# Kernel tuning notes

Hardware: AMD Instinct MI355X
Metric: run time of the kernel (lower is better)

Reference implementation:

```python
import jax, jax.numpy as jnp
import numpy as np

F_IN, F_H, N_A, N_B = 256, 512, 40, 4
N_GRAPHS, NODES_PER_GRAPH = 4096, 32
N_NODES = N_GRAPHS * NODES_PER_GRAPH
D_OUT = N_B + N_B * N_A  # 164
BN_EPS = 1e-5


def setup_inputs() -> dict:
    key = jax.random.key(0)
    ks = jax.random.split(key, 8)
    X = jax.random.normal(ks[0], (N_NODES, F_IN), dtype=jnp.float32)
    # fixed-size graphs: consistent NX / NX_rep pair
    NX = jnp.full((N_GRAPHS,), NODES_PER_GRAPH, dtype=jnp.int64)
    NX_rep = jnp.repeat(jnp.arange(N_GRAPHS, dtype=jnp.int64), NODES_PER_GRAPH)
    def kaiming(k, fo, fi):
        return jax.random.normal(k, (fo, fi), dtype=jnp.float32) * np.float32(1.0 / np.sqrt(fi))
    return {
        "X": X, "NX": NX, "NX_rep": NX_rep,
        "W_h": kaiming(ks[1], F_H, 2 * F_IN),          # linear_h (no bias)
        "g_h": jnp.ones((F_H,), jnp.float32), "b_h": jnp.zeros((F_H,), jnp.float32),
        "W_ht": kaiming(ks[2], F_H, F_IN),              # linear_h_t (no bias)
        "g_ht": jnp.ones((F_H,), jnp.float32), "b_ht": jnp.zeros((F_H,), jnp.float32),
        "W_x": kaiming(ks[3], D_OUT, F_H) * 0.1,        # linear_x
        "b_x": jnp.zeros((D_OUT,), jnp.float32),
        "W_xt": kaiming(ks[4], 1, F_H) * 0.1,           # linear_x_t
        "b_xt": jnp.zeros((1,), jnp.float32),
    }


def _batchnorm(x, gamma, beta):
    # BatchNorm1d in training mode: batch statistics, biased variance
    mean = jnp.mean(x, axis=0)
    var = jnp.var(x, axis=0)
    return (x - mean) * jax.lax.rsqrt(var + BN_EPS) * gamma + beta


def reference(X, NX, NX_rep, W_h, g_h, b_h, W_ht, g_ht, b_ht, W_x, b_x, W_xt, b_xt):
    n_graphs = NX.shape[0]
    # graph-level mean pooling via segment sum  -> [G, F_in]
    X_end = jax.ops.segment_sum(X, NX_rep, num_segments=n_graphs) / NX[:, None].astype(X.dtype)
    # concat node features with gathered graph context -> [N, 2*F_in]
    Xc = jnp.concatenate([X, X_end[NX_rep]], axis=1)
    X_h = jax.nn.relu(_batchnorm(Xc @ W_h.T, g_h, b_h))          # [N, F_h]
    X_h_end = jax.nn.relu(_batchnorm(X_end @ W_ht.T, g_ht, b_ht))  # [G, F_h]
    X_x = jnp.exp(X_h @ W_x.T + b_x)                              # [N, D_OUT]
    X_x_end = jnp.exp(X_h_end @ W_xt.T + b_xt)                    # [G, 1]
    # segmented softmax denominator (per graph, over all nodes x D_OUT + end logit)
    X_sum = jnp.sum(jax.ops.segment_sum(X_x, NX_rep, num_segments=n_graphs),
                    axis=-1, keepdims=True) + X_x_end             # [G, 1]
    X_softmax = X_x / X_sum[NX_rep]                               # [N, D_OUT]
    X_softmax_end = X_x_end / X_sum                               # [G, 1]
    connect = X_softmax[:, :N_B]                                  # [N, N_B]
    append = X_softmax[:, N_B:].reshape(-1, N_A, N_B)             # [N, N_A, N_B]
    end = X_softmax_end.squeeze(-1)                               # [G]
    return (append, connect, end)
```

## Files before the change

### kernel.cpp

```cpp
#include <hip/hip_runtime.h>
#include <hip/hip_bf16.h>

typedef __hip_bfloat16 bf16;
typedef __attribute__((ext_vector_type(8))) short bf16x8;
typedef __attribute__((ext_vector_type(4))) float f32x4;

#define N_NODES   131072
#define N_GRAPHS  4096
#define FIN       256
#define FH        512
#define NPAD      176
#define NREAL     164

#define OFF_XENDB  0UL
#define OFF_W1A    2097152UL
#define OFF_BCAT   2359296UL
#define OFF_WXB    2883584UL
#define OFF_STATS  3063808UL
#define OFF_XXE    3072000UL
#define OFF_CCAT   3088384UL
#define OFF_H      19865600UL

__device__ __forceinline__ void gld_lds16(const void* g, void* l) {
  __builtin_amdgcn_global_load_lds(
      (const __attribute__((address_space(1))) void*)g,
      (__attribute__((address_space(3))) void*)l, 16, 0, 0);
}

__device__ __forceinline__ float bf2f(unsigned short u) {
  unsigned int x = ((unsigned int)u) << 16; float f;
  __builtin_memcpy(&f, &x, 4); return f;
}
__device__ __forceinline__ unsigned short f2bf(float f) {
  bf16 h = __float2bfloat16(f); unsigned short u;
  __builtin_memcpy(&u, &h, 2); return u;
}

__global__ __launch_bounds__(256) void k_wcast(
    const float* __restrict__ W_h, const float* __restrict__ W_ht,
    const float* __restrict__ W_x,
    bf16* __restrict__ W1a, bf16* __restrict__ Bcat, bf16* __restrict__ Wxb,
    float* __restrict__ stats)
{
  int i = blockIdx.x * 256 + threadIdx.x;
  if (i < 2048) stats[i] = 0.f;
  if (i < 512 * 512) {
    int of = i >> 9, ic = i & 511;
    float v = W_h[i];
    if (ic < 256) W1a[of * 256 + ic] = __float2bfloat16(v);
    else          Bcat[of * 256 + (ic - 256)] = __float2bfloat16(v);
  }
  if (i < 512 * 256) Bcat[512 * 256 + i] = __float2bfloat16(W_ht[i]);
  if (i < NPAD * 512) {
    int n = i >> 9;
    Wxb[i] = (n < NREAL) ? __float2bfloat16(W_x[i]) : __float2bfloat16(0.f);
  }
}

__global__ __launch_bounds__(256) void k_xend(
    const float* __restrict__ X, const int* __restrict__ NX,
    bf16* __restrict__ X_endb)
{
  int g = blockIdx.x;
  int t = threadIdx.x;
  int cg = t & 63;
  int rg = t >> 6;
  const float* Xg = X + (long)g * 32 * FIN;
  float4 s = {0.f, 0.f, 0.f, 0.f};
  #pragma unroll
  for (int r = 0; r < 8; ++r) {
    float4 v = *(const float4*)(Xg + (rg * 8 + r) * FIN + cg * 4);
    s.x += v.x; s.y += v.y; s.z += v.z; s.w += v.w;
  }
  __shared__ float4 red[256];
  red[t] = s;
  __syncthreads();
  if (t < 64) {
    float4 a = red[t], b = red[t + 64], c = red[t + 128], d = red[t + 192];
    float inv = 1.f / (float)NX[g];
    float4 m = {(a.x + b.x + c.x + d.x) * inv, (a.y + b.y + c.y + d.y) * inv,
                (a.z + b.z + c.z + d.z) * inv, (a.w + b.w + c.w + d.w) * inv};
    ushort4 u = {f2bf(m.x), f2bf(m.y), f2bf(m.z), f2bf(m.w)};
    *(ushort4*)(X_endb + (long)g * FIN + t * 4) = u;
  }
}

__global__ __launch_bounds__(256, 2) void gemm0(
    const bf16* __restrict__ A, const bf16* __restrict__ B,
    float* __restrict__ Cout, float* __restrict__ s1e, float* __restrict__ s2e)
{
  const int bid = blockIdx.x;
  const int blkM = bid >> 3, blkN = bid & 7;
  const int tid = threadIdx.x;
  const int w = tid >> 6, lane = tid & 63;
  const int wm = w >> 1, wn = w & 1;

  __shared__ __align__(16) bf16 lA[128 * 32];
  __shared__ __align__(16) bf16 lB[128 * 32];
  __shared__ float sred[2][2][128];

  f32x4 acc[4][4] = {};
  const int rS = lane >> 2;
  const int cS = (lane & 3) * 8;
  const long baseA = (long)blkM * 128;
  const long baseB = (long)blkN * 128;

  for (int kk = 0; kk < FIN; kk += 32) {
    #pragma unroll
    for (int c = 0; c < 2; ++c) {
      int chunk = 2 * w + c;
      gld_lds16(A + (baseA + chunk * 16 + rS) * FIN + kk + cS, &lA[chunk * 16 * 32]);
      gld_lds16(B + (baseB + chunk * 16 + rS) * FIN + kk + cS, &lB[chunk * 16 * 32]);
    }
    __syncthreads();
    bf16x8 a8[4], b8[4];
    #pragma unroll
    for (int t = 0; t < 4; ++t) {
      a8[t] = *(const bf16x8*)&lA[(wm * 64 + t * 16 + (lane & 15)) * 32 + (lane >> 4) * 8];
      b8[t] = *(const bf16x8*)&lB[(wn * 64 + t * 16 + (lane & 15)) * 32 + (lane >> 4) * 8];
    }
    #pragma unroll
    for (int tm = 0; tm < 4; ++tm)
      #pragma unroll
      for (int tn = 0; tn < 4; ++tn)
        acc[tm][tn] = __builtin_amdgcn_mfma_f32_16x16x32_bf16(a8[tm], b8[tn], acc[tm][tn], 0, 0, 0);
    __syncthreads();
  }

  const int rowq = (lane >> 4) * 4;
  const int coll = lane & 15;
  float p1[4] = {0.f, 0.f, 0.f, 0.f}, p2[4] = {0.f, 0.f, 0.f, 0.f};
  #pragma unroll
  for (int tm = 0; tm < 4; ++tm)
    #pragma unroll
    for (int tn = 0; tn < 4; ++tn)
      #pragma unroll
      for (int r = 0; r < 4; ++r) {
        long row = baseA + wm * 64 + tm * 16 + rowq + r;
        int col = (int)baseB + wn * 64 + tn * 16 + coll;
        float v = acc[tm][tn][r];
        Cout[row * 1024 + col] = v;
        p1[tn] += v; p2[tn] += v * v;
      }

  if (blkN >= 4) {
    #pragma unroll
    for (int tn = 0; tn < 4; ++tn) {
      float q1 = p1[tn], q2 = p2[tn];
      q1 += __shfl_xor(q1, 16); q1 += __shfl_xor(q1, 32);
      q2 += __shfl_xor(q2, 16); q2 += __shfl_xor(q2, 32);
      if (lane < 16) {
        sred[wm][0][wn * 64 + tn * 16 + lane] = q1;
        sred[wm][1][wn * 64 + tn * 16 + lane] = q2;
      }
    }
    __syncthreads();
    int st = tid >> 7, c = tid & 127;
    float v = sred[0][st][c] + sred[1][st][c];
    atomicAdd((st ? s2e : s1e) + (blkN - 4) * 128 + c, v);
  }
}

__global__ __launch_bounds__(256) void k_xxend(
    const float* __restrict__ Ccat, const float* __restrict__ s1e,
    const float* __restrict__ s2e, const float* __restrict__ g_ht,
    const float* __restrict__ b_ht, const float* __restrict__ Wxt,
    const float* __restrict__ bxt, float* __restrict__ Xxe)
{
  __shared__ float aL[512], cL[512];
  int tid = threadIdx.x;
  #pragma unroll
  for (int i = tid; i < 512; i += 256) {
    float mean = s1e[i] * 2.44140625e-4f;
    float var = s2e[i] * 2.44140625e-4f - mean * mean;
    float a = g_ht[i] / sqrtf(var + 1e-5f);
    aL[i] = a; cL[i] = b_ht[i] - mean * a;
  }
  __syncthreads();
  int w = tid >> 6, lane = tid & 63;
  int g = blockIdx.x * 4 + w;
  const float* h = Ccat + (long)g * 1024 + 512;
  float acc = 0.f;
  #pragma unroll
  for (int i = 0; i < 8; ++i) {
    int j = lane + i * 64;
    float x = fmaxf(aL[j] * h[j] + cL[j], 0.f);
    acc += x * Wxt[j];
  }
  #pragma unroll
  for (int off = 32; off; off >>= 1) acc += __shfl_xor(acc, off);
  if (lane == 0) Xxe[g] = expf(acc + bxt[0]);
}

__global__ __launch_bounds__(256, 2) void gemm1(
    const float* __restrict__ X, const bf16* __restrict__ W1a,
    const float* __restrict__ Ccat, bf16* __restrict__ H,
    float* __restrict__ s1m, float* __restrict__ s2m)
{
  const int bid = blockIdx.x;
  const int blkM = bid >> 2, blkN = bid & 3;
  const int tid = threadIdx.x;
  const int w = tid >> 6, lane = tid & 63;
  const int wm = w >> 1, wn = w & 1;

  __shared__ __align__(16) bf16 lA[128 * 32];
  __shared__ __align__(16) bf16 lB[128 * 32];
  __shared__ float sred[2][2][128];

  f32x4 acc[4][4] = {};
  const int rS = lane >> 2;
  const int cS = (lane & 3) * 8;
  const long baseA = (long)blkM * 128;
  const long baseB = (long)blkN * 128;

  for (int kk = 0; kk < FIN; kk += 32) {
    #pragma unroll
    for (int c = 0; c < 2; ++c) {
      int chunk = 2 * w + c;
      gld_lds16(W1a + (baseB + chunk * 16 + rS) * FIN + kk + cS, &lB[chunk * 16 * 32]);
    }
    #pragma unroll
    for (int c = 0; c < 2; ++c) {
      int chunk = 2 * w + c;
      const float* src = X + (baseA + chunk * 16 + rS) * FIN + kk + cS;
      float4 v0 = *(const float4*)src;
      float4 v1 = *(const float4*)(src + 4);
      ushort4 u0 = {f2bf(v0.x), f2bf(v0.y), f2bf(v0.z), f2bf(v0.w)};
      ushort4 u1 = {f2bf(v1.x), f2bf(v1.y), f2bf(v1.z), f2bf(v1.w)};
      uint4 pk; __builtin_memcpy(&pk, &u0, 8); __builtin_memcpy(((char*)&pk) + 8, &u1, 8);
      *(uint4*)&lA[(chunk * 16 + rS) * 32 + cS] = pk;
    }
    __syncthreads();
    bf16x8 a8[4], b8[4];
    #pragma unroll
    for (int t = 0; t < 4; ++t) {
      a8[t] = *(const bf16x8*)&lA[(wm * 64 + t * 16 + (lane & 15)) * 32 + (lane >> 4) * 8];
      b8[t] = *(const bf16x8*)&lB[(wn * 64 + t * 16 + (lane & 15)) * 32 + (lane >> 4) * 8];
    }
    #pragma unroll
    for (int tm = 0; tm < 4; ++tm)
      #pragma unroll
      for (int tn = 0; tn < 4; ++tn)
        acc[tm][tn] = __builtin_amdgcn_mfma_f32_16x16x32_bf16(a8[tm], b8[tn], acc[tm][tn], 0, 0, 0);
    __syncthreads();
  }

  const int rowq = (lane >> 4) * 4;
  const int coll = lane & 15;
  float p1[4] = {0.f, 0.f, 0.f, 0.f}, p2[4] = {0.f, 0.f, 0.f, 0.f};
  #pragma unroll
  for (int tm = 0; tm < 4; ++tm)
    #pragma unroll
    for (int tn = 0; tn < 4; ++tn)
      #pragma unroll
      for (int r = 0; r < 4; ++r) {
        long row = baseA + wm * 64 + tm * 16 + rowq + r;
        int col = (int)baseB + wn * 64 + tn * 16 + coll;
        int g = (int)(row >> 5);
        float h = acc[tm][tn][r] + Ccat[(long)g * 1024 + col];
        H[row * FH + col] = __float2bfloat16(h);
        p1[tn] += h; p2[tn] += h * h;
      }

  #pragma unroll
  for (int tn = 0; tn < 4; ++tn) {
    float q1 = p1[tn], q2 = p2[tn];
    q1 += __shfl_xor(q1, 16); q1 += __shfl_xor(q1, 32);
    q2 += __shfl_xor(q2, 16); q2 += __shfl_xor(q2, 32);
    if (lane < 16) {
      sred[wm][0][wn * 64 + tn * 16 + lane] = q1;
      sred[wm][1][wn * 64 + tn * 16 + lane] = q2;
    }
  }
  __syncthreads();
  int st = tid >> 7, c = tid & 127;
  float v = sred[0][st][c] + sred[1][st][c];
  atomicAdd((st ? s2m : s1m) + (int)baseB + c, v);
}

__global__ __launch_bounds__(256, 2) void gemm2(
    const bf16* __restrict__ Hraw, const bf16* __restrict__ Wxb,
    const float* __restrict__ s1m, const float* __restrict__ s2m,
    const float* __restrict__ g_h, const float* __restrict__ b_h,
    const float* __restrict__ b_x, const float* __restrict__ Xxe,
    float* __restrict__ outA, float* __restrict__ outC, float* __restrict__ outE)
{
  const int blk = blockIdx.x;
  const int tid = threadIdx.x;
  const int w = tid >> 6, lane = tid & 63;

  __shared__ __align__(16) bf16 lA[128 * 32];
  __shared__ __align__(16) bf16 lB[NPAD * 32];
  __shared__ float aL[512], cL[512];

  #pragma unroll
  for (int i = tid; i < 512; i += 256) {
    float mean = s1m[i] * 7.62939453125e-6f;
    float var = s2m[i] * 7.62939453125e-6f - mean * mean;
    float a = g_h[i] / sqrtf(var + 1e-5f);
    aL[i] = a; cL[i] = b_h[i] - mean * a;
  }
  __syncthreads();

  f32x4 acc[2][11] = {};
  const int rS = lane >> 2;
  const int cS = (lane & 3) * 8;
  const long baseRow = (long)blk * 128;

  for (int kk = 0; kk < FH; kk += 32) {
    for (int o = w; o < 11; o += 4)
      gld_lds16(Wxb + (o * 16 + rS) * FH + kk + cS, &lB[o * 16 * 32]);

    f32x4 a0 = *(const f32x4*)&aL[kk + cS];
    f32x4 a1 = *(const f32x4*)&aL[kk + cS + 4];
    f32x4 c0 = *(const f32x4*)&cL[kk + cS];
    f32x4 c1 = *(const f32x4*)&cL[kk + cS + 4];
    #pragma unroll
    for (int c = 0; c < 2; ++c) {
      int chunk = 2 * w + c;
      uint4 raw = *(const uint4*)(Hraw + (baseRow + chunk * 16 + rS) * FH + kk + cS);
      unsigned short* u = (unsigned short*)&raw;
      #pragma unroll
      for (int j = 0; j < 4; ++j) {
        float v = bf2f(u[j]);
        u[j] = f2bf(fmaxf(a0[j] * v + c0[j], 0.f));
      }
      #pragma unroll
      for (int j = 0; j < 4; ++j) {
        float v = bf2f(u[4 + j]);
        u[4 + j] = f2bf(fmaxf(a1[j] * v + c1[j], 0.f));
      }
      *(uint4*)&lA[(chunk * 16 + rS) * 32 + cS] = raw;
    }
    __syncthreads();

    bf16x8 a8[2], b8[11];
    #pragma unroll
    for (int t = 0; t < 2; ++t)
      a8[t] = *(const bf16x8*)&lA[(w * 32 + t * 16 + (lane & 15)) * 32 + (lane >> 4) * 8];
    #pragma unroll
    for (int t = 0; t < 11; ++t)
      b8[t] = *(const bf16x8*)&lB[(t * 16 + (lane & 15)) * 32 + (lane >> 4) * 8];
    #pragma unroll
    for (int tm = 0; tm < 2; ++tm)
      #pragma unroll
      for (int tn = 0; tn < 11; ++tn)
        acc[tm][tn] = __builtin_amdgcn_mfma_f32_16x16x32_bf16(a8[tm], b8[tn], acc[tm][tn], 0, 0, 0);
    __syncthreads();
  }

  const int rowq = (lane >> 4) * 4;
  const int coll = lane & 15;
  const int g = blk * 4 + w;
  float psum = 0.f;
  #pragma unroll
  for (int tn = 0; tn < 11; ++tn) {
    int col = tn * 16 + coll;
    bool valid = col < NREAL;
    float bx = valid ? b_x[col] : 0.f;
    #pragma unroll
    for (int tm = 0; tm < 2; ++tm)
      #pragma unroll
      for (int r = 0; r < 4; ++r) {
        float p = valid ? expf(acc[tm][tn][r] + bx) : 0.f;
        acc[tm][tn][r] = p;
        psum += p;
      }
  }
  #pragma unroll
  for (int off = 32; off; off >>= 1) psum += __shfl_xor(psum, off);
  float Xe = Xxe[g];
  float inv = 1.0f / (psum + Xe);
  if (lane == 0) outE[g] = Xe * inv;

  #pragma unroll
  for (int tn = 0; tn < 11; ++tn) {
    int col = tn * 16 + coll;
    if (col >= NREAL) continue;
    #pragma unroll
    for (int tm = 0; tm < 2; ++tm)
      #pragma unroll
      for (int r = 0; r < 4; ++r) {
        long row = baseRow + w * 32 + tm * 16 + rowq + r;
        float v = acc[tm][tn][r] * inv;
        if (col >= 4) outA[row * 160 + (col - 4)] = v;
        else          outC[row * 4 + col] = v;
      }
  }
}

extern "C" void kernel_launch(void* const* d_in, const int* in_sizes, int n_in,
                              void* d_out, int out_size, void* d_ws, size_t ws_size,
                              hipStream_t stream)
{
  const float* X    = (const float*)d_in[0];
  const int*   NX   = (const int*)d_in[1];
  const float* W_h  = (const float*)d_in[3];
  const float* g_h  = (const float*)d_in[4];
  const float* b_h  = (const float*)d_in[5];
  const float* W_ht = (const float*)d_in[6];
  const float* g_ht = (const float*)d_in[7];
  const float* b_ht = (const float*)d_in[8];
  const float* W_x  = (const float*)d_in[9];
  const float* b_x  = (const float*)d_in[10];
  const float* W_xt = (const float*)d_in[11];
  const float* b_xt = (const float*)d_in[12];

  char* ws = (char*)d_ws;
  bf16*  X_endb= (bf16*)(ws + OFF_XENDB);
  bf16*  W1a   = (bf16*)(ws + OFF_W1A);
  bf16*  Bcat  = (bf16*)(ws + OFF_BCAT);
  bf16*  Wxb   = (bf16*)(ws + OFF_WXB);
  float* stats = (float*)(ws + OFF_STATS);
  float* s1m = stats, *s2m = stats + 512, *s1e = stats + 1024, *s2e = stats + 1536;
  float* Xxe   = (float*)(ws + OFF_XXE);
  float* Ccat  = (float*)(ws + OFF_CCAT);
  bf16*  H     = (bf16*)(ws + OFF_H);

  float* outA = (float*)d_out;
  float* outC = outA + (long)N_NODES * 160;
  float* outE = outC + (long)N_NODES * 4;

  k_wcast<<<1024, 256, 0, stream>>>(W_h, W_ht, W_x, W1a, Bcat, Wxb, stats);
  k_xend<<<N_GRAPHS, 256, 0, stream>>>(X, NX, X_endb);
  gemm0<<<256, 256, 0, stream>>>(X_endb, Bcat, Ccat, s1e, s2e);
  k_xxend<<<1024, 256, 0, stream>>>(Ccat, s1e, s2e, g_ht, b_ht, W_xt, b_xt, Xxe);
  gemm1<<<4096, 256, 0, stream>>>(X, W1a, Ccat, H, s1m, s2m);
  gemm2<<<1024, 256, 0, stream>>>(H, Wxb, s1m, s2m, g_h, b_h, b_x, Xxe, outA, outC, outE);
}
```

Before: 427.6 us.

## Pre-cast X to bf16 in pooling kernel and widen gemm1 tile to full N

The pooling kernel now also writes a bf16 copy of X, so gemm1 loads bf16 activations directly via global_load_lds instead of re-reading and converting fp32 X. gemm1 now computes 64 rows by all 512 columns per block, so each X row is read once rather than once per N-block. Batch-norm statistics go straight to global atomics per wave, with no LDS reduction. Costs are a 64MB workspace write, more accumulator registers and LDS per block, and heavier atomic contention on the stats.

```diff
diff --git a/kernel.cpp b/kernel.cpp
--- a/kernel.cpp
+++ b/kernel.cpp
@@ -12,14 +12,15 @@
 #define NPAD      176
 #define NREAL     164
 
-#define OFF_XENDB  0UL
-#define OFF_W1A    2097152UL
-#define OFF_BCAT   2359296UL
-#define OFF_WXB    2883584UL
-#define OFF_STATS  3063808UL
-#define OFF_XXE    3072000UL
-#define OFF_CCAT   3088384UL
-#define OFF_H      19865600UL
+#define OFF_XB     0UL
+#define OFF_XENDB  67108864UL
+#define OFF_W1A    69206016UL
+#define OFF_BCAT   69468160UL
+#define OFF_WXB    69992448UL
+#define OFF_STATS  70172672UL
+#define OFF_XXE    70180864UL
+#define OFF_CCAT   70197248UL
+#define OFF_H      86974464UL
 
 __device__ __forceinline__ void gld_lds16(const void* g, void* l) {
   __builtin_amdgcn_global_load_lds(
@@ -59,18 +60,22 @@
 
 __global__ __launch_bounds__(256) void k_xend(
     const float* __restrict__ X, const int* __restrict__ NX,
-    bf16* __restrict__ X_endb)
+    bf16* __restrict__ Xb, bf16* __restrict__ X_endb)
 {
   int g = blockIdx.x;
   int t = threadIdx.x;
   int cg = t & 63;
   int rg = t >> 6;
   const float* Xg = X + (long)g * 32 * FIN;
+  bf16* Xbg = Xb + (long)g * 32 * FIN;
   float4 s = {0.f, 0.f, 0.f, 0.f};
   #pragma unroll
   for (int r = 0; r < 8; ++r) {
-    float4 v = *(const float4*)(Xg + (rg * 8 + r) * FIN + cg * 4);
+    int off = (rg * 8 + r) * FIN + cg * 4;
+    float4 v = *(const float4*)(Xg + off);
     s.x += v.x; s.y += v.y; s.z += v.z; s.w += v.w;
+    ushort4 u = {f2bf(v.x), f2bf(v.y), f2bf(v.z), f2bf(v.w)};
+    *(ushort4*)(Xbg + off) = u;
   }
   __shared__ float4 red[256];
   red[t] = s;
@@ -193,89 +198,81 @@
 }
 
 __global__ __launch_bounds__(256, 2) void gemm1(
-    const float* __restrict__ X, const bf16* __restrict__ W1a,
+    const bf16* __restrict__ Xb, const bf16* __restrict__ W1a,
     const float* __restrict__ Ccat, bf16* __restrict__ H,
     float* __restrict__ s1m, float* __restrict__ s2m)
 {
   const int bid = blockIdx.x;
-  const int blkM = bid >> 2, blkN = bid & 3;
   const int tid = threadIdx.x;
   const int w = tid >> 6, lane = tid & 63;
-  const int wm = w >> 1, wn = w & 1;
-
-  __shared__ __align__(16) bf16 lA[128 * 32];
-  __shared__ __align__(16) bf16 lB[128 * 32];
-  __shared__ float sred[2][2][128];
-
-  f32x4 acc[4][4] = {};
+
+  __shared__ __align__(16) bf16 lA[64 * 32];
+  __shared__ __align__(16) bf16 lB[512 * 32];
+
+  f32x4 acc[4][8] = {};
   const int rS = lane >> 2;
   const int cS = (lane & 3) * 8;
-  const long baseA = (long)blkM * 128;
-  const long baseB = (long)blkN * 128;
+  const long baseA = (long)bid * 64;
 
   for (int kk = 0; kk < FIN; kk += 32) {
-    #pragma unroll
-    for (int c = 0; c < 2; ++c) {
-      int chunk = 2 * w + c;
-      gld_lds16(W1a + (baseB + chunk * 16 + rS) * FIN + kk + cS, &lB[chunk * 16 * 32]);
-    }
-    #pragma unroll
-    for (int c = 0; c < 2; ++c) {
-      int chunk = 2 * w + c;
-      const float* src = X + (baseA + chunk * 16 + rS) * FIN + kk + cS;
-      float4 v0 = *(const float4*)src;
-      float4 v1 = *(const float4*)(src + 4);
-      ushort4 u0 = {f2bf(v0.x), f2bf(v0.y), f2bf(v0.z), f2bf(v0.w)};
-      ushort4 u1 = {f2bf(v1.x), f2bf(v1.y), f2bf(v1.z), f2bf(v1.w)};
-      uint4 pk; __builtin_memcpy(&pk, &u0, 8); __builtin_memcpy(((char*)&pk) + 8, &u1, 8);
-      *(uint4*)&lA[(chunk * 16 + rS) * 32 + cS] = pk;
-    }
-    __syncthreads();
-    bf16x8 a8[4], b8[4];
-    #pragma unroll
-    for (int t = 0; t < 4; ++t) {
-      a8[t] = *(const bf16x8*)&lA[(wm * 64 + t * 16 + (lane & 15)) * 32 + (lane >> 4) * 8];
-      b8[t] = *(const bf16x8*)&lB[(wn * 64 + t * 16 + (lane & 15)) * 32 + (lane >> 4) * 8];
-    }
-    #pragma unroll
-    for (int tm = 0; tm < 4; ++tm)
-      #pragma unroll
-      for (int tn = 0; tn < 4; ++tn)
-        acc[tm][tn] = __builtin_amdgcn_mfma_f32_16x16x32_bf16(a8[tm], b8[tn], acc[tm][tn], 0, 0, 0);
-    __syncthreads();
-  }
-
-  const int rowq = (lane >> 4) * 4;
+    gld_lds16(Xb + (baseA + w * 16 + rS) * FIN + kk + cS, &lA[w * 16 * 32]);
+    #pragma unroll
+    for (int o = 0; o < 8; ++o) {
+      int chunk = o * 4 + w;
+      gld_lds16(W1a + (chunk * 16 + rS) * FIN + kk + cS, &lB[chunk * 16 * 32]);
+    }
+    __syncthreads();
+    bf16x8 a8[4], b8[8];
+    #pragma unroll
+    for (int t = 0; t < 4; ++t)
+      a8[t] = *(const bf16x8*)&lA[(t * 16 + (lane & 15)) * 32 + (lane >> 4) * 8];
+    #pragma unroll
+    for (int j = 0; j < 8; ++j)
+      b8[j] = *(const bf16x8*)&lB[(w * 128 + j * 16 + (lane & 15)) * 32 + (lane >> 4) * 8];
+    #pragma unroll
+    for (int t = 0; t < 4; ++t)
+      #pragma unroll
+      for (int j = 0; j < 8; ++j)
+        acc[t][j] = __builtin_amdgcn_mfma_f32_16x16x32_bf16(a8[t], b8[j], acc[t][j], 0, 0, 0);
+    __syncthreads();
+  }
+
+  const int q4 = (lane >> 4) * 4;
   const int coll = lane & 15;
-  float p1[4] = {0.f, 0.f, 0.f, 0.f}, p2[4] = {0.f, 0.f, 0.f, 0.f};
-  #pragma unroll
-  for (int tm = 0; tm < 4; ++tm)
-    #pragma unroll
-    for (int tn = 0; tn < 4; ++tn)
+  float ct[2][8];
+  #pragma unroll
+  for (int a = 0; a < 2; ++a)
+    #pragma unroll
+    for (int j = 0; j < 8; ++j)
+      ct[a][j] = Ccat[(long)(bid * 2 + a) * 1024 + w * 128 + j * 16 + coll];
+
+  float p1[8], p2[8];
+  #pragma unroll
+  for (int j = 0; j < 8; ++j) { p1[j] = 0.f; p2[j] = 0.f; }
+
+  #pragma unroll
+  for (int t = 0; t < 4; ++t)
+    #pragma unroll
+    for (int j = 0; j < 8; ++j)
       #pragma unroll
       for (int r = 0; r < 4; ++r) {
-        long row = baseA + wm * 64 + tm * 16 + rowq + r;
-        int col = (int)baseB + wn * 64 + tn * 16 + coll;
-        int g = (int)(row >> 5);
-        float h = acc[tm][tn][r] + Ccat[(long)g * 1024 + col];
+        long row = baseA + t * 16 + q4 + r;
+        int col = w * 128 + j * 16 + coll;
+        float h = acc[t][j][r] + ct[t >> 1][j];
         H[row * FH + col] = __float2bfloat16(h);
-        p1[tn] += h; p2[tn] += h * h;
-      }
-
-  #pragma unroll
-  for (int tn = 0; tn < 4; ++tn) {
-    float q1 = p1[tn], q2 = p2[tn];
+        p1[j] += h; p2[j] += h * h;
+      }
+
+  #pragma unroll
+  for (int j = 0; j < 8; ++j) {
+    float q1 = p1[j], q2 = p2[j];
     q1 += __shfl_xor(q1, 16); q1 += __shfl_xor(q1, 32);
     q2 += __shfl_xor(q2, 16); q2 += __shfl_xor(q2, 32);
     if (lane < 16) {
-      sred[wm][0][wn * 64 + tn * 16 + lane] = q1;
-      sred[wm][1][wn * 64 + tn * 16 + lane] = q2;
-    }
-  }
-  __syncthreads();
-  int st = tid >> 7, c = tid & 127;
-  float v = sred[0][st][c] + sred[1][st][c];
-  atomicAdd((st ? s2m : s1m) + (int)baseB + c, v);
+      atomicAdd(s1m + w * 128 + j * 16 + lane, q1);
+      atomicAdd(s2m + w * 128 + j * 16 + lane, q2);
+    }
+  }
 }
 
 __global__ __launch_bounds__(256, 2) void gemm2(
@@ -407,6 +404,7 @@
   const float* b_xt = (const float*)d_in[12];
 
   char* ws = (char*)d_ws;
+  bf16*  Xb    = (bf16*)(ws + OFF_XB);
   bf16*  X_endb= (bf16*)(ws + OFF_XENDB);
   bf16*  W1a   = (bf16*)(ws + OFF_W1A);
   bf16*  Bcat  = (bf16*)(ws + OFF_BCAT);
@@ -422,9 +420,9 @@
   float* outE = outC + (long)N_NODES * 4;
 
   k_wcast<<<1024, 256, 0, stream>>>(W_h, W_ht, W_x, W1a, Bcat, Wxb, stats);
-  k_xend<<<N_GRAPHS, 256, 0, stream>>>(X, NX, X_endb);
+  k_xend<<<N_GRAPHS, 256, 0, stream>>>(X, NX, Xb, X_endb);
   gemm0<<<256, 256, 0, stream>>>(X_endb, Bcat, Ccat, s1e, s2e);
   k_xxend<<<1024, 256, 0, stream>>>(Ccat, s1e, s2e, g_ht, b_ht, W_xt, b_xt, Xxe);
-  gemm1<<<4096, 256, 0, stream>>>(X, W1a, Ccat, H, s1m, s2m);
+  gemm1<<<2048, 256, 0, stream>>>(Xb, W1a, Ccat, H, s1m, s2m);
   gemm2<<<1024, 256, 0, stream>>>(H, Wxb, s1m, s2m, g_h, b_h, b_x, Xxe, outA, outC, outE);
 }
```

After: 403.1 us. 1.06x faster.
